# Performance work log

Measured on AMD Instinct MI355X. Metric: run time of the kernel, lower is better.

## Reference

```python
import jax, jax.numpy as jnp
import numpy as np

B, S, D, H = 2, 2048, 1024, 16
HD = D // H
FF = 4 * D
EPS = 1e-5


def _ln(x, g, b):
    mu = jnp.mean(x, axis=-1, keepdims=True)
    var = jnp.var(x, axis=-1, keepdims=True)
    return (x - mu) * jax.lax.rsqrt(var + EPS) * g + b


def setup_inputs() -> dict:
    key = jax.random.key(0)
    ks = jax.random.split(key, 8)
    std = 0.02
    inp = {
        'x': jax.random.normal(ks[0], (B, S, D), jnp.float32),
        'mask': jnp.ones((B, S), jnp.int32),
        'Wq': jax.random.normal(ks[1], (D, D), jnp.float32) * std,
        'bq': jnp.zeros((D,), jnp.float32),
        'Wk': jax.random.normal(ks[2], (D, D), jnp.float32) * std,
        'bk': jnp.zeros((D,), jnp.float32),
        'Wv': jax.random.normal(ks[3], (D, D), jnp.float32) * std,
        'bv': jnp.zeros((D,), jnp.float32),
        'Wo': jax.random.normal(ks[4], (D, D), jnp.float32) * std,
        'bo': jnp.zeros((D,), jnp.float32),
        'W1': jax.random.normal(ks[5], (D, FF), jnp.float32) * std,
        'b1': jnp.zeros((FF,), jnp.float32),
        'W2': jax.random.normal(ks[6], (FF, D), jnp.float32) * std,
        'b2': jnp.zeros((D,), jnp.float32),
        'g1': jnp.ones((D,), jnp.float32),
        'be1': jnp.zeros((D,), jnp.float32),
        'g2': jnp.ones((D,), jnp.float32),
        'be2': jnp.zeros((D,), jnp.float32),
    }
    return inp


def reference(x, mask, Wq, bq, Wk, bk, Wv, bv, Wo, bo, W1, b1, W2, b2, g1, be1, g2, be2):
    # multi-head attention (dropout in eval mode => identity)
    q = (x @ Wq + bq).reshape(B, S, H, HD).transpose(0, 2, 1, 3)  # [B,H,S,HD]
    k = (x @ Wk + bk).reshape(B, S, H, HD).transpose(0, 2, 1, 3)
    v = (x @ Wv + bv).reshape(B, S, H, HD).transpose(0, 2, 1, 3)
    scores = jnp.einsum('bhqd,bhkd->bhqk', q, k) / jnp.sqrt(jnp.float32(HD))
    m = mask[:, None, None, :]  # [B,1,1,S] broadcast over queries
    scores = jnp.where(m == 0, jnp.float32(-1e9), scores)
    attn = jax.nn.softmax(scores, axis=-1)
    ao = jnp.einsum('bhqk,bhkd->bhqd', attn, v).transpose(0, 2, 1, 3).reshape(B, S, D)
    attn_out = ao @ Wo + bo
    x1 = _ln(x + attn_out, g1, be1)
    ffn = jax.nn.relu(x1 @ W1 + b1) @ W2 + b2
    return _ln(x1 + ffn, g2, be2)
```

## Files before the change

kernel.cpp:

```cpp
#include <hip/hip_runtime.h>
#include <stdint.h>
#include <stddef.h>

#define B_ 2
#define S_ 2048
#define D_ 1024
#define H_ 16
#define HD_ 64
#define FF_ 4096

typedef unsigned short u16;
typedef __attribute__((ext_vector_type(8))) short bf16x8;
typedef __attribute__((ext_vector_type(4))) float f32x4;

__device__ __forceinline__ u16 f2bf(float f) {
  unsigned u = __float_as_uint(f);
  u += 0x7fffu + ((u >> 16) & 1u);
  return (u16)(u >> 16);
}

__device__ __forceinline__ f32x4 mfma16(bf16x8 a, bf16x8 b, f32x4 c) {
  return __builtin_amdgcn_mfma_f32_16x16x32_bf16(a, b, c, 0, 0, 0);
}

__device__ __forceinline__ void gload16(const void* g, void* l) {
  __builtin_amdgcn_global_load_lds(
      (const __attribute__((address_space(1))) void*)g,
      (__attribute__((address_space(3))) void*)l, 16, 0, 0);
}

__global__ __launch_bounds__(256) void cvt_kernel(const float* __restrict__ src,
                                                  u16* __restrict__ dst, int n) {
  int i = (blockIdx.x * 256 + threadIdx.x) * 4;
  if (i >= n) return;
  float4 v = *(const float4*)(src + i);
  ushort4 o = { f2bf(v.x), f2bf(v.y), f2bf(v.z), f2bf(v.w) };
  *(ushort4*)(dst + i) = o;
}

__global__ __launch_bounds__(256) void transpose_cvt_kernel(
    const float* __restrict__ W, u16* __restrict__ WT, int K, int N) {
  __shared__ u16 t[32][33];
  int k0 = blockIdx.x * 32;
  int n0 = blockIdx.y * 32;
  int tid = threadIdx.x;
  int r = tid >> 3;
  int c = (tid & 7) << 2;
  float4 v = *(const float4*)(W + (size_t)(k0 + r) * N + n0 + c);
  t[r][c + 0] = f2bf(v.x); t[r][c + 1] = f2bf(v.y);
  t[r][c + 2] = f2bf(v.z); t[r][c + 3] = f2bf(v.w);
  __syncthreads();
  ushort4 o;
  o.x = t[c + 0][r]; o.y = t[c + 1][r]; o.z = t[c + 2][r]; o.w = t[c + 3][r];
  *(ushort4*)(WT + (size_t)(n0 + r) * K + k0 + c) = o;
}

__global__ __launch_bounds__(256) void gemm_bt_relu(
    const u16* __restrict__ A, const u16* __restrict__ BT,
    const float* __restrict__ bias, u16* __restrict__ outp,
    int M, int N, int K) {
  __shared__ __align__(16) u16 As[128 * 32];
  __shared__ __align__(16) u16 Bs[128 * 32];
  int tid = threadIdx.x;
  int lane = tid & 63;
  int wave = tid >> 6;
  int quad = lane >> 4;
  int l16 = lane & 15;
  int m0 = blockIdx.x * 128;
  int n0 = blockIdx.y * 128;
  int wm = (wave >> 1) * 64;
  int wn = (wave & 1) * 64;

  f32x4 zero = {0.f, 0.f, 0.f, 0.f};
  f32x4 acc[4][4];
#pragma unroll
  for (int i = 0; i < 4; i++)
#pragma unroll
    for (int j = 0; j < 4; j++) acc[i][j] = zero;

  int c0 = tid, c1 = tid + 256;
  const u16* ga0 = A + (size_t)(m0 + (c0 >> 2)) * K + (c0 & 3) * 8;
  const u16* ga1 = A + (size_t)(m0 + (c1 >> 2)) * K + (c1 & 3) * 8;
  const u16* gb0 = BT + (size_t)(n0 + (c0 >> 2)) * K + (c0 & 3) * 8;
  const u16* gb1 = BT + (size_t)(n0 + (c1 >> 2)) * K + (c1 & 3) * 8;

  for (int k0 = 0; k0 < K; k0 += 32) {
    gload16(ga0 + k0, &As[c0 * 8]);
    gload16(ga1 + k0, &As[c1 * 8]);
    gload16(gb0 + k0, &Bs[c0 * 8]);
    gload16(gb1 + k0, &Bs[c1 * 8]);
    __syncthreads();
    bf16x8 af[4], bfr[4];
#pragma unroll
    for (int i = 0; i < 4; i++)
      af[i] = *(const bf16x8*)&As[(wm + i * 16 + l16) * 32 + quad * 8];
#pragma unroll
    for (int j = 0; j < 4; j++)
      bfr[j] = *(const bf16x8*)&Bs[(wn + j * 16 + l16) * 32 + quad * 8];
#pragma unroll
    for (int i = 0; i < 4; i++)
#pragma unroll
      for (int j = 0; j < 4; j++)
        acc[i][j] = mfma16(af[i], bfr[j], acc[i][j]);
    __syncthreads();
  }

#pragma unroll
  for (int j = 0; j < 4; j++) {
    int gcol = n0 + wn + j * 16 + l16;
    float bv = bias[gcol];
#pragma unroll
    for (int i = 0; i < 4; i++) {
#pragma unroll
      for (int r = 0; r < 4; r++) {
        int grow = m0 + wm + i * 16 + quad * 4 + r;
        float val = acc[i][j][r] + bv;
        outp[(size_t)grow * N + gcol] = f2bf(val > 0.f ? val : 0.f);
      }
    }
  }
}

__global__ __launch_bounds__(256) void gemm_bt_sk2(
    const u16* __restrict__ A, const u16* __restrict__ BT,
    const float* __restrict__ bias, float* __restrict__ outp,
    int M, int N, int K, int Kc) {
  __shared__ __align__(16) u16 As[128 * 32];
  __shared__ __align__(16) u16 Bs[128 * 32];
  int tid = threadIdx.x;
  int lane = tid & 63;
  int wave = tid >> 6;
  int quad = lane >> 4;
  int l16 = lane & 15;
  int m0 = blockIdx.x * 128;
  int n0 = blockIdx.y * 128;
  int kb = blockIdx.z * Kc;
  int wm = (wave >> 1) * 64;
  int wn = (wave & 1) * 64;

  f32x4 zero = {0.f, 0.f, 0.f, 0.f};
  f32x4 acc[4][4];
#pragma unroll
  for (int i = 0; i < 4; i++)
#pragma unroll
    for (int j = 0; j < 4; j++) acc[i][j] = zero;

  int c0 = tid, c1 = tid + 256;
  const u16* ga0 = A + (size_t)(m0 + (c0 >> 2)) * K + (c0 & 3) * 8 + kb;
  const u16* ga1 = A + (size_t)(m0 + (c1 >> 2)) * K + (c1 & 3) * 8 + kb;
  const u16* gb0 = BT + (size_t)(n0 + (c0 >> 2)) * K + (c0 & 3) * 8 + kb;
  const u16* gb1 = BT + (size_t)(n0 + (c1 >> 2)) * K + (c1 & 3) * 8 + kb;

  for (int k0 = 0; k0 < Kc; k0 += 32) {
    gload16(ga0 + k0, &As[c0 * 8]);
    gload16(ga1 + k0, &As[c1 * 8]);
    gload16(gb0 + k0, &Bs[c0 * 8]);
    gload16(gb1 + k0, &Bs[c1 * 8]);
    __syncthreads();
    bf16x8 af[4], bfr[4];
#pragma unroll
    for (int i = 0; i < 4; i++)
      af[i] = *(const bf16x8*)&As[(wm + i * 16 + l16) * 32 + quad * 8];
#pragma unroll
    for (int j = 0; j < 4; j++)
      bfr[j] = *(const bf16x8*)&Bs[(wn + j * 16 + l16) * 32 + quad * 8];
#pragma unroll
    for (int i = 0; i < 4; i++)
#pragma unroll
      for (int j = 0; j < 4; j++)
        acc[i][j] = mfma16(af[i], bfr[j], acc[i][j]);
    __syncthreads();
  }

  float* outz = outp + (size_t)blockIdx.z * M * N;
  float biasmul = (blockIdx.z == 0) ? 1.f : 0.f;
#pragma unroll
  for (int j = 0; j < 4; j++) {
    int gcol = n0 + wn + j * 16 + l16;
    float bv = bias[gcol] * biasmul;
#pragma unroll
    for (int i = 0; i < 4; i++) {
#pragma unroll
      for (int r = 0; r < 4; r++) {
        int grow = m0 + wm + i * 16 + quad * 4 + r;
        outz[(size_t)grow * N + gcol] = acc[i][j][r] + bv;
      }
    }
  }
}

__global__ __launch_bounds__(256) void gemm_qkv(
    const u16* __restrict__ A, const u16* __restrict__ BT,
    const float* __restrict__ bq, const float* __restrict__ bk,
    const float* __restrict__ bvp,
    u16* __restrict__ qb, u16* __restrict__ kb, u16* __restrict__ vb) {
  const int K = 1024;
  __shared__ __align__(16) u16 As[128 * 32];
  __shared__ __align__(16) u16 Bs[128 * 32];
  int tid = threadIdx.x;
  int lane = tid & 63;
  int wave = tid >> 6;
  int quad = lane >> 4;
  int l16 = lane & 15;
  int m0 = blockIdx.x * 128;
  int n0 = blockIdx.y * 128;
  int wm = (wave >> 1) * 64;
  int wn = (wave & 1) * 64;

  f32x4 zero = {0.f, 0.f, 0.f, 0.f};
  f32x4 acc[4][4];
#pragma unroll
  for (int i = 0; i < 4; i++)
#pragma unroll
    for (int j = 0; j < 4; j++) acc[i][j] = zero;

  int c0 = tid, c1 = tid + 256;
  const u16* ga0 = A + (size_t)(m0 + (c0 >> 2)) * K + (c0 & 3) * 8;
  const u16* ga1 = A + (size_t)(m0 + (c1 >> 2)) * K + (c1 & 3) * 8;
  const u16* gb0 = BT + (size_t)(n0 + (c0 >> 2)) * K + (c0 & 3) * 8;
  const u16* gb1 = BT + (size_t)(n0 + (c1 >> 2)) * K + (c1 & 3) * 8;

  for (int k0 = 0; k0 < K; k0 += 32) {
    gload16(ga0 + k0, &As[c0 * 8]);
    gload16(ga1 + k0, &As[c1 * 8]);
    gload16(gb0 + k0, &Bs[c0 * 8]);
    gload16(gb1 + k0, &Bs[c1 * 8]);
    __syncthreads();
    bf16x8 af[4], bfr[4];
#pragma unroll
    for (int i = 0; i < 4; i++)
      af[i] = *(const bf16x8*)&As[(wm + i * 16 + l16) * 32 + quad * 8];
#pragma unroll
    for (int j = 0; j < 4; j++)
      bfr[j] = *(const bf16x8*)&Bs[(wn + j * 16 + l16) * 32 + quad * 8];
#pragma unroll
    for (int i = 0; i < 4; i++)
#pragma unroll
      for (int j = 0; j < 4; j++)
        acc[i][j] = mfma16(af[i], bfr[j], acc[i][j]);
    __syncthreads();
  }

  int region = n0 >> 10;
  const float* bias = region == 0 ? bq : (region == 1 ? bk : bvp);
  u16* outp = region == 0 ? qb : (region == 1 ? kb : vb);
  float scale = region == 0 ? 0.125f * 1.4426950408889634f : 1.f;

#pragma unroll
  for (int j = 0; j < 4; j++) {
    int gcol = (n0 & 1023) + wn + j * 16 + l16;
    float bv = bias[gcol];
    int h = gcol >> 6, hd = gcol & 63;
#pragma unroll
    for (int i = 0; i < 4; i++) {
#pragma unroll
      for (int r = 0; r < 4; r++) {
        int grow = m0 + wm + i * 16 + quad * 4 + r;
        float val = (acc[i][j][r] + bv) * scale;
        int b = grow >> 11, s = grow & 2047;
        if (region < 2) {
          outp[(((size_t)(b * H_ + h)) * S_ + s) * HD_ + hd] = f2bf(val);
        } else {
          outp[(((size_t)(b * H_ + h)) * HD_ + hd) * S_ + s] = f2bf(val);
        }
      }
    }
  }
}

__global__ __launch_bounds__(256, 4) void attn_kernel(
    const u16* __restrict__ q, const u16* __restrict__ k,
    const u16* __restrict__ vt, const int* __restrict__ mask,
    u16* __restrict__ ao) {
  __shared__ __align__(16) u16 Ks[64 * 72];
  __shared__ __align__(16) u16 Vs[64 * 72];
  __shared__ __align__(16) u16 Ps[4][16 * 72];
  int tid = threadIdx.x;
  int lane = tid & 63;
  int wave = tid >> 6;
  int quad = lane >> 4;
  int l16 = lane & 15;
  int bh = blockIdx.y;
  int b = bh >> 4;
  int h = bh & 15;
  int qrow0 = blockIdx.x * 64 + wave * 16;

  const u16* qh = q + (size_t)bh * S_ * HD_;
  const u16* kh = k + (size_t)bh * S_ * HD_;
  const u16* vh = vt + (size_t)bh * HD_ * S_;

  bf16x8 qf0 = *(const bf16x8*)(qh + (size_t)(qrow0 + l16) * HD_ + quad * 8);
  bf16x8 qf1 = *(const bf16x8*)(qh + (size_t)(qrow0 + l16) * HD_ + 32 + quad * 8);

  int sr = tid >> 3, sc = tid & 7;
  const u16* kg0 = kh + sr * HD_ + sc * 8;
  const u16* kg1 = kh + (sr + 32) * HD_ + sc * 8;
  const u16* vg0 = vh + (size_t)sr * S_ + sc * 8;
  const u16* vg1 = vh + (size_t)(sr + 32) * S_ + sc * 8;
  int kr0 = (sr & 1) * 16 + (sr >> 1);
  int ko0 = kr0 * 72 + sc * 8;
  int ko1 = (32 + kr0) * 72 + sc * 8;
  int vo0 = sr * 72 + sc * 8;
  int vo1 = (sr + 32) * 72 + sc * 8;
  const int* mrow = mask + b * S_ + 2 * l16;

  float l_part[4] = {0.f, 0.f, 0.f, 0.f};
  f32x4 zero = {0.f, 0.f, 0.f, 0.f};
  f32x4 o_acc[4];
#pragma unroll
  for (int c = 0; c < 4; c++) o_acc[c] = zero;

  u16* pw = &Ps[wave][0];

  for (int kt = 0; kt < S_; kt += 64) {
    bf16x8 kv0 = *(const bf16x8*)(kg0 + (size_t)kt * HD_);
    bf16x8 kv1 = *(const bf16x8*)(kg1 + (size_t)kt * HD_);
    bf16x8 vv0 = *(const bf16x8*)(vg0 + kt);
    bf16x8 vv1 = *(const bf16x8*)(vg1 + kt);
    int2 mk0 = *(const int2*)(mrow + kt);
    int2 mk1 = *(const int2*)(mrow + kt + 32);

    __syncthreads();
    *(bf16x8*)&Ks[ko0] = kv0;
    *(bf16x8*)&Ks[ko1] = kv1;
    *(bf16x8*)&Vs[vo0] = vv0;
    *(bf16x8*)&Vs[vo1] = vv1;
    __syncthreads();

#pragma unroll
    for (int g = 0; g < 2; g++) {
      int2 mk = g == 0 ? mk0 : mk1;
      f32x4 se, so;
      {
        int rowb = (g * 32 + l16) * 72;
        bf16x8 e0 = *(const bf16x8*)&Ks[rowb + quad * 8];
        bf16x8 e1 = *(const bf16x8*)&Ks[rowb + 32 + quad * 8];
        se = mfma16(qf1, e1, mfma16(qf0, e0, zero));
      }
      {
        int rowb = (g * 32 + 16 + l16) * 72;
        bf16x8 o0 = *(const bf16x8*)&Ks[rowb + quad * 8];
        bf16x8 o1 = *(const bf16x8*)&Ks[rowb + 32 + quad * 8];
        so = mfma16(qf1, o1, mfma16(qf0, o0, zero));
      }
#pragma unroll
      for (int r = 0; r < 4; r++) {
        float e0 = exp2f(se[r]);
        float e1 = exp2f(so[r]);
        float p0 = mk.x ? e0 : 0.f;
        float p1 = mk.y ? e1 : 0.f;
        l_part[r] += p0 + p1;
        unsigned pk = __builtin_amdgcn_perm(__float_as_uint(p1),
                                            __float_as_uint(p0), 0x07060302u);
        *(unsigned*)&pw[(quad * 4 + r) * 72 + g * 32 + 2 * l16] = pk;
      }
    }
    bf16x8 pf0 = *(const bf16x8*)&pw[l16 * 72 + quad * 8];
    bf16x8 pf1 = *(const bf16x8*)&pw[l16 * 72 + 32 + quad * 8];
#pragma unroll
    for (int c = 0; c < 4; c++) {
      bf16x8 vf0 = *(const bf16x8*)&Vs[(c * 16 + l16) * 72 + quad * 8];
      bf16x8 vf1 = *(const bf16x8*)&Vs[(c * 16 + l16) * 72 + 32 + quad * 8];
      o_acc[c] = mfma16(pf0, vf0, o_acc[c]);
      o_acc[c] = mfma16(pf1, vf1, o_acc[c]);
    }
  }

#pragma unroll
  for (int r = 0; r < 4; r++) {
    float s = l_part[r];
#pragma unroll
    for (int off = 1; off < 16; off <<= 1) s += __shfl_xor(s, off);
    float inv = 1.f / s;
    int srow = qrow0 + quad * 4 + r;
#pragma unroll
    for (int c = 0; c < 4; c++) {
      float val = o_acc[c][r] * inv;
      ao[((size_t)(b * S_ + srow)) * D_ + h * HD_ + c * 16 + l16] = f2bf(val);
    }
  }
}

__global__ __launch_bounds__(256) void ln_kernel(
    const float* __restrict__ xa, const float* __restrict__ add0,
    const float* __restrict__ add1,
    const float* __restrict__ g, const float* __restrict__ be,
    float* __restrict__ outf, u16* __restrict__ outb) {
  int row = blockIdx.x;
  int tid = threadIdx.x;
  int lane = tid & 63;
  int wv = tid >> 6;
  const float4 a = *(const float4*)(xa + (size_t)row * D_ + tid * 4);
  const float4 c = *(const float4*)(add0 + (size_t)row * D_ + tid * 4);
  const float4 d = *(const float4*)(add1 + (size_t)row * D_ + tid * 4);
  float v0 = a.x + c.x + d.x, v1 = a.y + c.y + d.y;
  float v2 = a.z + c.z + d.z, v3 = a.w + c.w + d.w;
  float s = v0 + v1 + v2 + v3;
  float sq = v0 * v0 + v1 * v1 + v2 * v2 + v3 * v3;
#pragma unroll
  for (int off = 1; off < 64; off <<= 1) {
    s += __shfl_xor(s, off);
    sq += __shfl_xor(sq, off);
  }
  __shared__ float red[8];
  if (lane == 0) { red[wv] = s; red[4 + wv] = sq; }
  __syncthreads();
  s = red[0] + red[1] + red[2] + red[3];
  sq = red[4] + red[5] + red[6] + red[7];
  float mean = s * (1.f / D_);
  float var = sq * (1.f / D_) - mean * mean;
  float rstd = rsqrtf(var + 1e-5f);
  const float4 gv = *(const float4*)(g + tid * 4);
  const float4 bv = *(const float4*)(be + tid * 4);
  float y0 = (v0 - mean) * rstd * gv.x + bv.x;
  float y1 = (v1 - mean) * rstd * gv.y + bv.y;
  float y2 = (v2 - mean) * rstd * gv.z + bv.z;
  float y3 = (v3 - mean) * rstd * gv.w + bv.w;
  float4 o = {y0, y1, y2, y3};
  *(float4*)(outf + (size_t)row * D_ + tid * 4) = o;
  if (outb) {
    ushort4 ob = {f2bf(y0), f2bf(y1), f2bf(y2), f2bf(y3)};
    *(ushort4*)(outb + (size_t)row * D_ + tid * 4) = ob;
  }
}

extern "C" void kernel_launch(void* const* d_in, const int* in_sizes, int n_in,
                              void* d_out, int out_size, void* d_ws, size_t ws_size,
                              hipStream_t stream) {
  const float* x = (const float*)d_in[0];
  const int* mask = (const int*)d_in[1];
  const float* Wq = (const float*)d_in[2];
  const float* bq = (const float*)d_in[3];
  const float* Wk = (const float*)d_in[4];
  const float* bk = (const float*)d_in[5];
  const float* Wv = (const float*)d_in[6];
  const float* bv = (const float*)d_in[7];
  const float* Wo = (const float*)d_in[8];
  const float* bo = (const float*)d_in[9];
  const float* W1 = (const float*)d_in[10];
  const float* b1 = (const float*)d_in[11];
  const float* W2 = (const float*)d_in[12];
  const float* b2 = (const float*)d_in[13];
  const float* g1 = (const float*)d_in[14];
  const float* be1 = (const float*)d_in[15];
  const float* g2 = (const float*)d_in[16];
  const float* be2 = (const float*)d_in[17];

  const size_t MB = 1ull << 20;
  char* ws = (char*)d_ws;
  u16* wTq = (u16*)(ws + 0 * MB);
  u16* wTk = (u16*)(ws + 2 * MB);
  u16* wTv = (u16*)(ws + 4 * MB);
  u16* wTo = (u16*)(ws + 6 * MB);
  u16* w1T = (u16*)(ws + 8 * MB);
  u16* w2T = (u16*)(ws + 16 * MB);
  u16* xb  = (u16*)(ws + 24 * MB);
  u16* qb  = (u16*)(ws + 32 * MB);
  u16* kb  = (u16*)(ws + 40 * MB);
  u16* vb  = (u16*)(ws + 48 * MB);
  u16* ao  = (u16*)(ws + 56 * MB);
  float* proj = (float*)(ws + 64 * MB);
  float* x1f  = (float*)(ws + 24 * MB);
  u16*   x1b  = (u16*)(ws + 40 * MB);
  u16*   h1   = (u16*)(ws + 96 * MB);
  float* ffn2 = (float*)(ws + 48 * MB);

  cvt_kernel<<<dim3((B_ * S_ * D_) / 1024), dim3(256), 0, stream>>>(x, xb, B_ * S_ * D_);
  transpose_cvt_kernel<<<dim3(32, 32), dim3(256), 0, stream>>>(Wq, wTq, D_, D_);
  transpose_cvt_kernel<<<dim3(32, 32), dim3(256), 0, stream>>>(Wk, wTk, D_, D_);
  transpose_cvt_kernel<<<dim3(32, 32), dim3(256), 0, stream>>>(Wv, wTv, D_, D_);
  transpose_cvt_kernel<<<dim3(32, 32), dim3(256), 0, stream>>>(Wo, wTo, D_, D_);
  transpose_cvt_kernel<<<dim3(32, 128), dim3(256), 0, stream>>>(W1, w1T, D_, FF_);
  transpose_cvt_kernel<<<dim3(128, 32), dim3(256), 0, stream>>>(W2, w2T, FF_, D_);

  gemm_qkv<<<dim3(32, 24), dim3(256), 0, stream>>>(xb, wTq, bq, bk, bv, qb, kb, vb);

  attn_kernel<<<dim3(S_ / 64, B_ * H_), dim3(256), 0, stream>>>(qb, kb, vb, mask, ao);

  gemm_bt_sk2<<<dim3(32, 8, 2), dim3(256), 0, stream>>>(ao, wTo, bo, proj, 4096, 1024, 1024, 512);

  ln_kernel<<<dim3(4096), dim3(256), 0, stream>>>(
      x, proj, proj + (size_t)4096 * 1024, g1, be1, x1f, x1b);

  gemm_bt_relu<<<dim3(32, 32), dim3(256), 0, stream>>>(x1b, w1T, b1, h1, 4096, 4096, 1024);

  gemm_bt_sk2<<<dim3(32, 8, 2), dim3(256), 0, stream>>>(h1, w2T, b2, ffn2, 4096, 1024, 4096, 2048);

  ln_kernel<<<dim3(4096), dim3(256), 0, stream>>>(
      x1f, ffn2, ffn2 + (size_t)4096 * 1024, g2, be2, (float*)d_out, (u16*)nullptr);
}
```

Measured before the change: 406.9 us.

## Double attention query rows per wave and swizzle GEMM tiles across XCDs

Each attention wave now handles 32 query rows (two 16-row groups) instead of 16, so every K/V tile staged in shared memory serves twice as many queries and the attention grid is halved. The GEMM kernels also remap block indices so that consecutive M tiles land on the same XCD, aiming for better L2 reuse of A/B tiles. The changes cost more registers and a larger P buffer in the attention kernel, which may reduce occupancy, and leave half as many attention blocks to spread across the CUs.

```diff
diff --git a/kernel.cpp b/kernel.cpp
--- a/kernel.cpp
+++ b/kernel.cpp
@@ -27,6 +27,20 @@
   __builtin_amdgcn_global_load_lds(
       (const __attribute__((address_space(1))) void*)g,
       (__attribute__((address_space(3))) void*)l, 16, 0, 0);
+}
+
+__device__ __forceinline__ void swizzle_mn(int& mt, int& nt) {
+  int gm = gridDim.x;
+  if ((gm & 7) == 0) {
+    int bid = blockIdx.y * gm + blockIdx.x;
+    int mper = gm >> 3;
+    int xcd = bid & 7, idx = bid >> 3;
+    mt = xcd * mper + (idx % mper);
+    nt = idx / mper;
+  } else {
+    mt = blockIdx.x;
+    nt = blockIdx.y;
+  }
 }
 
 __global__ __launch_bounds__(256) void cvt_kernel(const float* __restrict__ src,
@@ -66,8 +80,10 @@
   int wave = tid >> 6;
   int quad = lane >> 4;
   int l16 = lane & 15;
-  int m0 = blockIdx.x * 128;
-  int n0 = blockIdx.y * 128;
+  int mt, nt;
+  swizzle_mn(mt, nt);
+  int m0 = mt * 128;
+  int n0 = nt * 128;
   int wm = (wave >> 1) * 64;
   int wn = (wave & 1) * 64;
 
@@ -132,8 +148,10 @@
   int wave = tid >> 6;
   int quad = lane >> 4;
   int l16 = lane & 15;
-  int m0 = blockIdx.x * 128;
-  int n0 = blockIdx.y * 128;
+  int mt, nt;
+  swizzle_mn(mt, nt);
+  int m0 = mt * 128;
+  int n0 = nt * 128;
   int kb = blockIdx.z * Kc;
   int wm = (wave >> 1) * 64;
   int wn = (wave & 1) * 64;
@@ -202,8 +220,10 @@
   int wave = tid >> 6;
   int quad = lane >> 4;
   int l16 = lane & 15;
-  int m0 = blockIdx.x * 128;
-  int n0 = blockIdx.y * 128;
+  int mt, nt;
+  swizzle_mn(mt, nt);
+  int m0 = mt * 128;
+  int n0 = nt * 128;
   int wm = (wave >> 1) * 64;
   int wn = (wave & 1) * 64;
 
@@ -274,7 +294,7 @@
     u16* __restrict__ ao) {
   __shared__ __align__(16) u16 Ks[64 * 72];
   __shared__ __align__(16) u16 Vs[64 * 72];
-  __shared__ __align__(16) u16 Ps[4][16 * 72];
+  __shared__ __align__(16) u16 Ps[4][32 * 72];
   int tid = threadIdx.x;
   int lane = tid & 63;
   int wave = tid >> 6;
@@ -283,14 +303,16 @@
   int bh = blockIdx.y;
   int b = bh >> 4;
   int h = bh & 15;
-  int qrow0 = blockIdx.x * 64 + wave * 16;
+  int qrow0 = blockIdx.x * 128 + wave * 32;
 
   const u16* qh = q + (size_t)bh * S_ * HD_;
   const u16* kh = k + (size_t)bh * S_ * HD_;
   const u16* vh = vt + (size_t)bh * HD_ * S_;
 
-  bf16x8 qf0 = *(const bf16x8*)(qh + (size_t)(qrow0 + l16) * HD_ + quad * 8);
-  bf16x8 qf1 = *(const bf16x8*)(qh + (size_t)(qrow0 + l16) * HD_ + 32 + quad * 8);
+  bf16x8 qfA0 = *(const bf16x8*)(qh + (size_t)(qrow0 + l16) * HD_ + quad * 8);
+  bf16x8 qfA1 = *(const bf16x8*)(qh + (size_t)(qrow0 + l16) * HD_ + 32 + quad * 8);
+  bf16x8 qfB0 = *(const bf16x8*)(qh + (size_t)(qrow0 + 16 + l16) * HD_ + quad * 8);
+  bf16x8 qfB1 = *(const bf16x8*)(qh + (size_t)(qrow0 + 16 + l16) * HD_ + 32 + quad * 8);
 
   int sr = tid >> 3, sc = tid & 7;
   const u16* kg0 = kh + sr * HD_ + sc * 8;
@@ -304,11 +326,12 @@
   int vo1 = (sr + 32) * 72 + sc * 8;
   const int* mrow = mask + b * S_ + 2 * l16;
 
-  float l_part[4] = {0.f, 0.f, 0.f, 0.f};
+  float l_pA[4] = {0.f, 0.f, 0.f, 0.f};
+  float l_pB[4] = {0.f, 0.f, 0.f, 0.f};
   f32x4 zero = {0.f, 0.f, 0.f, 0.f};
-  f32x4 o_acc[4];
-#pragma unroll
-  for (int c = 0; c < 4; c++) o_acc[c] = zero;
+  f32x4 o_accA[4], o_accB[4];
+#pragma unroll
+  for (int c = 0; c < 4; c++) { o_accA[c] = zero; o_accB[c] = zero; }
 
   u16* pw = &Ps[wave][0];
 
@@ -330,53 +353,62 @@
 #pragma unroll
     for (int g = 0; g < 2; g++) {
       int2 mk = g == 0 ? mk0 : mk1;
-      f32x4 se, so;
-      {
-        int rowb = (g * 32 + l16) * 72;
-        bf16x8 e0 = *(const bf16x8*)&Ks[rowb + quad * 8];
-        bf16x8 e1 = *(const bf16x8*)&Ks[rowb + 32 + quad * 8];
-        se = mfma16(qf1, e1, mfma16(qf0, e0, zero));
+      int rowe = (g * 32 + l16) * 72;
+      int rowo = (g * 32 + 16 + l16) * 72;
+      bf16x8 e0 = *(const bf16x8*)&Ks[rowe + quad * 8];
+      bf16x8 e1 = *(const bf16x8*)&Ks[rowe + 32 + quad * 8];
+      bf16x8 o0 = *(const bf16x8*)&Ks[rowo + quad * 8];
+      bf16x8 o1 = *(const bf16x8*)&Ks[rowo + 32 + quad * 8];
+      f32x4 seA = mfma16(qfA1, e1, mfma16(qfA0, e0, zero));
+      f32x4 soA = mfma16(qfA1, o1, mfma16(qfA0, o0, zero));
+      f32x4 seB = mfma16(qfB1, e1, mfma16(qfB0, e0, zero));
+      f32x4 soB = mfma16(qfB1, o1, mfma16(qfB0, o0, zero));
+#pragma unroll
+      for (int r = 0; r < 4; r++) {
+        float pA0 = mk.x ? exp2f(seA[r]) : 0.f;
+        float pA1 = mk.y ? exp2f(soA[r]) : 0.f;
+        float pB0 = mk.x ? exp2f(seB[r]) : 0.f;
+        float pB1 = mk.y ? exp2f(soB[r]) : 0.f;
+        l_pA[r] += pA0 + pA1;
+        l_pB[r] += pB0 + pB1;
+        unsigned pkA = __builtin_amdgcn_perm(__float_as_uint(pA1),
+                                             __float_as_uint(pA0), 0x07060302u);
+        unsigned pkB = __builtin_amdgcn_perm(__float_as_uint(pB1),
+                                             __float_as_uint(pB0), 0x07060302u);
+        *(unsigned*)&pw[(quad * 4 + r) * 72 + g * 32 + 2 * l16] = pkA;
+        *(unsigned*)&pw[(16 + quad * 4 + r) * 72 + g * 32 + 2 * l16] = pkB;
       }
-      {
-        int rowb = (g * 32 + 16 + l16) * 72;
-        bf16x8 o0 = *(const bf16x8*)&Ks[rowb + quad * 8];
-        bf16x8 o1 = *(const bf16x8*)&Ks[rowb + 32 + quad * 8];
-        so = mfma16(qf1, o1, mfma16(qf0, o0, zero));
-      }
-#pragma unroll
-      for (int r = 0; r < 4; r++) {
-        float e0 = exp2f(se[r]);
-        float e1 = exp2f(so[r]);
-        float p0 = mk.x ? e0 : 0.f;
-        float p1 = mk.y ? e1 : 0.f;
-        l_part[r] += p0 + p1;
-        unsigned pk = __builtin_amdgcn_perm(__float_as_uint(p1),
-                                            __float_as_uint(p0), 0x07060302u);
-        *(unsigned*)&pw[(quad * 4 + r) * 72 + g * 32 + 2 * l16] = pk;
-      }
-    }
-    bf16x8 pf0 = *(const bf16x8*)&pw[l16 * 72 + quad * 8];
-    bf16x8 pf1 = *(const bf16x8*)&pw[l16 * 72 + 32 + quad * 8];
+    }
+    bf16x8 pfA0 = *(const bf16x8*)&pw[l16 * 72 + quad * 8];
+    bf16x8 pfA1 = *(const bf16x8*)&pw[l16 * 72 + 32 + quad * 8];
+    bf16x8 pfB0 = *(const bf16x8*)&pw[(16 + l16) * 72 + quad * 8];
+    bf16x8 pfB1 = *(const bf16x8*)&pw[(16 + l16) * 72 + 32 + quad * 8];
 #pragma unroll
     for (int c = 0; c < 4; c++) {
       bf16x8 vf0 = *(const bf16x8*)&Vs[(c * 16 + l16) * 72 + quad * 8];
       bf16x8 vf1 = *(const bf16x8*)&Vs[(c * 16 + l16) * 72 + 32 + quad * 8];
-      o_acc[c] = mfma16(pf0, vf0, o_acc[c]);
-      o_acc[c] = mfma16(pf1, vf1, o_acc[c]);
+      o_accA[c] = mfma16(pfA1, vf1, mfma16(pfA0, vf0, o_accA[c]));
+      o_accB[c] = mfma16(pfB1, vf1, mfma16(pfB0, vf0, o_accB[c]));
     }
   }
 
 #pragma unroll
   for (int r = 0; r < 4; r++) {
-    float s = l_part[r];
-#pragma unroll
-    for (int off = 1; off < 16; off <<= 1) s += __shfl_xor(s, off);
-    float inv = 1.f / s;
-    int srow = qrow0 + quad * 4 + r;
+    float sA = l_pA[r], sB = l_pB[r];
+#pragma unroll
+    for (int off = 1; off < 16; off <<= 1) {
+      sA += __shfl_xor(sA, off);
+      sB += __shfl_xor(sB, off);
+    }
+    float invA = 1.f / sA, invB = 1.f / sB;
+    int srowA = qrow0 + quad * 4 + r;
+    int srowB = qrow0 + 16 + quad * 4 + r;
 #pragma unroll
     for (int c = 0; c < 4; c++) {
-      float val = o_acc[c][r] * inv;
-      ao[((size_t)(b * S_ + srow)) * D_ + h * HD_ + c * 16 + l16] = f2bf(val);
+      ao[((size_t)(b * S_ + srowA)) * D_ + h * HD_ + c * 16 + l16] =
+          f2bf(o_accA[c][r] * invA);
+      ao[((size_t)(b * S_ + srowB)) * D_ + h * HD_ + c * 16 + l16] =
+          f2bf(o_accB[c][r] * invB);
     }
   }
 }
@@ -475,7 +507,7 @@
 
   gemm_qkv<<<dim3(32, 24), dim3(256), 0, stream>>>(xb, wTq, bq, bk, bv, qb, kb, vb);
 
-  attn_kernel<<<dim3(S_ / 64, B_ * H_), dim3(256), 0, stream>>>(qb, kb, vb, mask, ao);
+  attn_kernel<<<dim3(S_ / 128, B_ * H_), dim3(256), 0, stream>>>(qb, kb, vb, mask, ao);
 
   gemm_bt_sk2<<<dim3(32, 8, 2), dim3(256), 0, stream>>>(ao, wTo, bo, proj, 4096, 1024, 1024, 512);
 
```

Measured after the change: 408.2 us. About the same (+0.3%).
